# Performance work log

Hardware: AMD Instinct MI355X
Metric: run time of the kernel (lower is better)

## Reference

```python
import jax, jax.numpy as jnp
import numpy as np

N_NODES = 50000
N_EDGES = 800000
N_EVAL = 500000
D = 96


def _sage_conv(x, edge_index, W_l, W_r, b):
    # PyG SAGEConv with aggr='add':
    #   aggr_out[v] = sum_{(u->v) in edges} x[u]
    #   out = aggr_out @ W_l^T-equivalent + b + x @ W_r  (we store W as [in, out])
    src, dst = edge_index[0], edge_index[1]
    msgs = x[src]                                        # [E, d_in] irregular gather
    aggr = jax.ops.segment_sum(msgs, dst, num_segments=x.shape[0])  # [N, d_in]
    return aggr @ W_l + b + x @ W_r                      # [N, d_out]


def setup_inputs() -> dict:
    key = jax.random.key(0)
    ks = jax.random.split(key, 8)
    scale = 1.0 / np.sqrt(D)
    Features = jax.random.normal(ks[0], (N_NODES, D), dtype=jnp.float32)
    A = jax.random.randint(ks[1], (2, N_EDGES), 0, N_NODES, dtype=jnp.int64)
    E = jax.random.randint(ks[2], (2, N_EVAL), 0, N_NODES, dtype=jnp.int64)
    W1_l = jax.random.normal(ks[3], (D, D), dtype=jnp.float32) * scale
    W1_r = jax.random.normal(ks[4], (D, D), dtype=jnp.float32) * scale
    b1 = jnp.zeros((D,), dtype=jnp.float32)
    W2_l = jax.random.normal(ks[5], (D, D), dtype=jnp.float32) * scale
    W2_r = jax.random.normal(ks[6], (D, D), dtype=jnp.float32) * scale
    b2 = jnp.zeros((D,), dtype=jnp.float32)
    return {"Features": Features, "A": A, "E": E,
            "W1_l": W1_l, "W1_r": W1_r, "b1": b1,
            "W2_l": W2_l, "W2_r": W2_r, "b2": b2}


def reference(Features, A, E, W1_l, W1_r, b1, W2_l, W2_r, b2):
    h = _sage_conv(Features, A, W1_l, W1_r, b1)          # [N, hidden]
    h = jax.nn.relu(h)
    # dropout in eval mode = identity
    h = _sage_conv(h, A, W2_l, W2_r, b2)                 # [N, out]
    # edge scoring: gather src/dst embeddings, dot, sigmoid
    src = h[E[0]]                                        # [n_eval, out]
    dst = h[E[1]]                                        # [n_eval, out]
    return jax.nn.sigmoid(jnp.sum(src * dst, axis=-1))   # [n_eval]
```

## Files before the change

### kernel.cpp

```cpp
#include <hip/hip_runtime.h>
#include <math.h>

#define N_NODES 50000
#define N_EDGES 800000
#define N_EVAL  500000
#define CSTRIDE 16
#define MAXDEG  64
#define NB_GEMM ((N_NODES + 63) / 64)
#define NCHUNK  (N_NODES * 24)
#define NB_AGG4 1172
#define NSLOT_C 1173
#define HALF_EVAL (N_EVAL / 2)

__device__ __forceinline__ float4 f4add(float4 a, float4 b) {
    return make_float4(a.x + b.x, a.y + b.y, a.z + b.z, a.w + b.w);
}
__device__ __forceinline__ float4 f4fma(float s, float4 w, float4 a) {
    return make_float4(fmaf(s, w.x, a.x), fmaf(s, w.y, a.y),
                       fmaf(s, w.z, a.z), fmaf(s, w.w, a.w));
}
__device__ __forceinline__ float4 ld4(const float* p) {
    return *(const float4*)p;
}


__device__ __forceinline__ void bucket_role(int idx, const int* __restrict__ src,
                                            const int* __restrict__ dst,
                                            int* __restrict__ degS,
                                            unsigned short* __restrict__ bucket) {
    int t = idx * 256 + threadIdx.x;
    if (t < N_EDGES / 4) {
        int4 s = ((const int4*)src)[t];
        int4 d = ((const int4*)dst)[t];
        int r0 = atomicAdd(&degS[(size_t)d.x * CSTRIDE], 1);
        int r1 = atomicAdd(&degS[(size_t)d.y * CSTRIDE], 1);
        int r2 = atomicAdd(&degS[(size_t)d.z * CSTRIDE], 1);
        int r3 = atomicAdd(&degS[(size_t)d.w * CSTRIDE], 1);
        if (r0 < MAXDEG) bucket[(size_t)d.x * MAXDEG + r0] = (unsigned short)s.x;
        if (r1 < MAXDEG) bucket[(size_t)d.y * MAXDEG + r1] = (unsigned short)s.y;
        if (r2 < MAXDEG) bucket[(size_t)d.z * MAXDEG + r2] = (unsigned short)s.z;
        if (r3 < MAXDEG) bucket[(size_t)d.w * MAXDEG + r3] = (unsigned short)s.w;
    }
}

struct IdxL { int4 p0, p1, p2, p3; int deg; };

__device__ __forceinline__ IdxL idx_load(int v, const int* __restrict__ degS,
                                         const unsigned short* __restrict__ bucket) {
    IdxL L;
    const int4* bk4 = (const int4*)(bucket + (size_t)v * MAXDEG);
    L.deg = degS[(size_t)v * CSTRIDE];
    L.p0 = bk4[0]; L.p1 = bk4[1]; L.p2 = bk4[2]; L.p3 = bk4[3];
    return L;
}

__device__ __forceinline__ float4 aggr_gather(IdxL L, int v, int c,
        const float* __restrict__ x, const unsigned short* __restrict__ bucket) {
    const float* xp = x + c * 4;
    int deg = L.deg;
    if (deg > MAXDEG) deg = MAXDEG;
    int idx[32];
    idx[0]  = L.p0.x & 0xffff; idx[1]  = (int)((unsigned)L.p0.x >> 16);
    idx[2]  = L.p0.y & 0xffff; idx[3]  = (int)((unsigned)L.p0.y >> 16);
    idx[4]  = L.p0.z & 0xffff; idx[5]  = (int)((unsigned)L.p0.z >> 16);
    idx[6]  = L.p0.w & 0xffff; idx[7]  = (int)((unsigned)L.p0.w >> 16);
    idx[8]  = L.p1.x & 0xffff; idx[9]  = (int)((unsigned)L.p1.x >> 16);
    idx[10] = L.p1.y & 0xffff; idx[11] = (int)((unsigned)L.p1.y >> 16);
    idx[12] = L.p1.z & 0xffff; idx[13] = (int)((unsigned)L.p1.z >> 16);
    idx[14] = L.p1.w & 0xffff; idx[15] = (int)((unsigned)L.p1.w >> 16);
    idx[16] = L.p2.x & 0xffff; idx[17] = (int)((unsigned)L.p2.x >> 16);
    idx[18] = L.p2.y & 0xffff; idx[19] = (int)((unsigned)L.p2.y >> 16);
    idx[20] = L.p2.z & 0xffff; idx[21] = (int)((unsigned)L.p2.z >> 16);
    idx[22] = L.p2.w & 0xffff; idx[23] = (int)((unsigned)L.p2.w >> 16);
    idx[24] = L.p3.x & 0xffff; idx[25] = (int)((unsigned)L.p3.x >> 16);
    idx[26] = L.p3.y & 0xffff; idx[27] = (int)((unsigned)L.p3.y >> 16);
    idx[28] = L.p3.z & 0xffff; idx[29] = (int)((unsigned)L.p3.z >> 16);
    idx[30] = L.p3.w & 0xffff; idx[31] = (int)((unsigned)L.p3.w >> 16);

    const float4 z = make_float4(0.f, 0.f, 0.f, 0.f);
    float4 t0, t1, t2, t3, t4, t5, t6, t7, t8, t9, t10, t11, t12, t13, t14, t15;
    if (deg >= 16) {
        t0  = ld4(xp + (size_t)idx[0]  * 96);
        t1  = ld4(xp + (size_t)idx[1]  * 96);
        t2  = ld4(xp + (size_t)idx[2]  * 96);
        t3  = ld4(xp + (size_t)idx[3]  * 96);
        t4  = ld4(xp + (size_t)idx[4]  * 96);
        t5  = ld4(xp + (size_t)idx[5]  * 96);
        t6  = ld4(xp + (size_t)idx[6]  * 96);
        t7  = ld4(xp + (size_t)idx[7]  * 96);
        t8  = ld4(xp + (size_t)idx[8]  * 96);
        t9  = ld4(xp + (size_t)idx[9]  * 96);
        t10 = ld4(xp + (size_t)idx[10] * 96);
        t11 = ld4(xp + (size_t)idx[11] * 96);
        t12 = ld4(xp + (size_t)idx[12] * 96);
        t13 = ld4(xp + (size_t)idx[13] * 96);
        t14 = ld4(xp + (size_t)idx[14] * 96);
        t15 = ld4(xp + (size_t)idx[15] * 96);
    } else if (deg >= 8) {
        t0 = ld4(xp + (size_t)idx[0] * 96);
        t1 = ld4(xp + (size_t)idx[1] * 96);
        t2 = ld4(xp + (size_t)idx[2] * 96);
        t3 = ld4(xp + (size_t)idx[3] * 96);
        t4 = ld4(xp + (size_t)idx[4] * 96);
        t5 = ld4(xp + (size_t)idx[5] * 96);
        t6 = ld4(xp + (size_t)idx[6] * 96);
        t7 = ld4(xp + (size_t)idx[7] * 96);
        t8 = z; t9 = z; t10 = z; t11 = z; t12 = z; t13 = z; t14 = z; t15 = z;
        if (deg > 8)  t8  = ld4(xp + (size_t)idx[8]  * 96);
        if (deg > 9)  t9  = ld4(xp + (size_t)idx[9]  * 96);
        if (deg > 10) t10 = ld4(xp + (size_t)idx[10] * 96);
        if (deg > 11) t11 = ld4(xp + (size_t)idx[11] * 96);
        if (deg > 12) t12 = ld4(xp + (size_t)idx[12] * 96);
        if (deg > 13) t13 = ld4(xp + (size_t)idx[13] * 96);
        if (deg > 14) t14 = ld4(xp + (size_t)idx[14] * 96);
    } else {
        t0 = z; t1 = z; t2 = z; t3 = z; t4 = z; t5 = z; t6 = z; t7 = z;
        t8 = z; t9 = z; t10 = z; t11 = z; t12 = z; t13 = z; t14 = z; t15 = z;
        if (deg > 0) t0 = ld4(xp + (size_t)idx[0] * 96);
        if (deg > 1) t1 = ld4(xp + (size_t)idx[1] * 96);
        if (deg > 2) t2 = ld4(xp + (size_t)idx[2] * 96);
        if (deg > 3) t3 = ld4(xp + (size_t)idx[3] * 96);
        if (deg > 4) t4 = ld4(xp + (size_t)idx[4] * 96);
        if (deg > 5) t5 = ld4(xp + (size_t)idx[5] * 96);
        if (deg > 6) t6 = ld4(xp + (size_t)idx[6] * 96);
    }
    float4 a0 = f4add(f4add(f4add(t0, t1), f4add(t2, t3)),
                      f4add(f4add(t4, t5), f4add(t6, t7)));
    float4 a1 = f4add(f4add(f4add(t8, t9), f4add(t10, t11)),
                      f4add(f4add(t12, t13), f4add(t14, t15)));
    if (deg > 16) {
        float4 u0, u1, u2, u3, u4, u5, u6, u7;
        u0 = ld4(xp + (size_t)idx[16] * 96);
        u1 = z; u2 = z; u3 = z; u4 = z; u5 = z; u6 = z; u7 = z;
        if (deg > 17) u1 = ld4(xp + (size_t)idx[17] * 96);
        if (deg > 18) u2 = ld4(xp + (size_t)idx[18] * 96);
        if (deg > 19) u3 = ld4(xp + (size_t)idx[19] * 96);
        if (deg > 20) u4 = ld4(xp + (size_t)idx[20] * 96);
        if (deg > 21) u5 = ld4(xp + (size_t)idx[21] * 96);
        if (deg > 22) u6 = ld4(xp + (size_t)idx[22] * 96);
        if (deg > 23) u7 = ld4(xp + (size_t)idx[23] * 96);
        a0 = f4add(a0, f4add(f4add(u0, u1), f4add(u2, u3)));
        a1 = f4add(a1, f4add(f4add(u4, u5), f4add(u6, u7)));
    }
    if (deg > 24) {
        float4 u0, u1, u2, u3, u4, u5, u6, u7;
        u0 = ld4(xp + (size_t)idx[24] * 96);
        u1 = z; u2 = z; u3 = z; u4 = z; u5 = z; u6 = z; u7 = z;
        if (deg > 25) u1 = ld4(xp + (size_t)idx[25] * 96);
        if (deg > 26) u2 = ld4(xp + (size_t)idx[26] * 96);
        if (deg > 27) u3 = ld4(xp + (size_t)idx[27] * 96);
        if (deg > 28) u4 = ld4(xp + (size_t)idx[28] * 96);
        if (deg > 29) u5 = ld4(xp + (size_t)idx[29] * 96);
        if (deg > 30) u6 = ld4(xp + (size_t)idx[30] * 96);
        if (deg > 31) u7 = ld4(xp + (size_t)idx[31] * 96);
        a0 = f4add(a0, f4add(f4add(u0, u1), f4add(u2, u3)));
        a1 = f4add(a1, f4add(f4add(u4, u5), f4add(u6, u7)));
    }
    if (deg > 32) {
        const unsigned short* bk = bucket + (size_t)v * MAXDEG;
        for (int i = 32; i < deg; ++i)
            a0 = f4add(a0, ld4(xp + (size_t)bk[i] * 96));
    }
    return f4add(a0, a1);
}

__device__ __forceinline__ void aggr_role4(int slot, int stride256,
        const float* __restrict__ x, const int* __restrict__ degS,
        const unsigned short* __restrict__ bucket, float* __restrict__ out) {
    const int STR = stride256 * 256;
    int gt = slot * 256 + threadIdx.x;
    bool val = gt < NCHUNK;
    int v = 0, c = 0;
    IdxL L;
    if (val) {
        v = gt / 24; c = gt - v * 24;
        L = idx_load(v, degS, bucket);
    }
    #pragma unroll
    for (int k = 0; k < 4; ++k) {
        int gtn = gt + STR;
        bool valn = (k < 3) && (gtn < NCHUNK);
        int vn = 0, cn = 0;
        IdxL Ln;
        if (valn) {
            vn = gtn / 24; cn = gtn - vn * 24;
            Ln = idx_load(vn, degS, bucket);
        }
        if (val) {
            float4 r = aggr_gather(L, v, c, x, bucket);
            *(float4*)(out + (size_t)v * 96 + c * 4) = r;
        }
        gt = gtn; v = vn; c = cn; L = Ln; val = valn;
    }
}

__device__ __forceinline__ void selfgemm_role(int g, const float* __restrict__ X,
                                              const float* __restrict__ W96,
                                              const float* __restrict__ bias,
                                              float* __restrict__ S,
                                              float* __restrict__ Ws,
                                              float* __restrict__ xT) {
    const int tid = threadIdx.x;
    const int j   = tid & 31;
    const int ty  = tid >> 5;
    const int v0  = g * 64;

    float acc[8][3];
    float b0 = bias[j], b1 = bias[j + 32], b2 = bias[j + 64];
    #pragma unroll
    for (int r = 0; r < 8; ++r) { acc[r][0] = b0; acc[r][1] = b1; acc[r][2] = b2; }

    const int sr = tid >> 2;
    const int sc = tid & 3;
    int sv = v0 + sr; if (sv >= N_NODES) sv = N_NODES - 1;

    for (int kc = 0; kc < 6; ++kc) {
        const float* W = W96 + kc * (16 * 96);
        const int kbase = kc * 16;
        __syncthreads();
        *(float4*)(Ws + tid * 4) = ld4(W + tid * 4);
        if (tid < 128)
            *(float4*)(Ws + (tid + 256) * 4) = ld4(W + (tid + 256) * 4);
        {
            float4 a = ld4(X + (size_t)sv * 96 + kbase + sc * 4);
            int k0 = sc * 4;
            xT[(k0 + 0) * 68 + sr] = a.x;
            xT[(k0 + 1) * 68 + sr] = a.y;
            xT[(k0 + 2) * 68 + sr] = a.z;
            xT[(k0 + 3) * 68 + sr] = a.w;
        }
        __syncthreads();
        #pragma unroll 8
        for (int kk = 0; kk < 16; ++kk) {
            float w0 = Ws[kk * 96 + j];
            float w1 = Ws[kk * 96 + j + 32];
            float w2 = Ws[kk * 96 + j + 64];
            float4 xa = *(const float4*)(xT + kk * 68 + ty * 8);
            float4 xb = *(const float4*)(xT + kk * 68 + ty * 8 + 4);
#define ROWFMA(r, xv)                                   \
            acc[r][0] = fmaf(xv, w0, acc[r][0]);        \
            acc[r][1] = fmaf(xv, w1, acc[r][1]);        \
            acc[r][2] = fmaf(xv, w2, acc[r][2]);
            ROWFMA(0, xa.x) ROWFMA(1, xa.y) ROWFMA(2, xa.z) ROWFMA(3, xa.w)
            ROWFMA(4, xb.x) ROWFMA(5, xb.y) ROWFMA(6, xb.z) ROWFMA(7, xb.w)
#undef ROWFMA
        }
    }
    #pragma unroll
    for (int r = 0; r < 8; ++r) {
        int v = v0 + ty * 8 + r;
        if (v < N_NODES) {
            S[(size_t)v * 96 + j]      = acc[r][0];
            S[(size_t)v * 96 + j + 32] = acc[r][1];
            S[(size_t)v * 96 + j + 64] = acc[r][2];
        }
    }
}


__global__ __launch_bounds__(256, 4) void k_fusedA(const int* __restrict__ src,
                                                   const int* __restrict__ dst,
                                                   int* __restrict__ degS,
                                                   unsigned short* __restrict__ bucket,
                                                   const float* __restrict__ X,
                                                   const float* __restrict__ Wr,
                                                   const float* __restrict__ bias,
                                                   float* __restrict__ S) {
    __shared__ float Ws[16 * 96];
    __shared__ float xT[16 * 68];
    int b = blockIdx.x;
    if (b & 1) selfgemm_role(b >> 1, X, Wr, bias, S, Ws, xT);
    else       bucket_role(b >> 1, src, dst, degS, bucket);
}

__global__ __launch_bounds__(256, 4) void k_aggr(const float* __restrict__ x,
                                                 const int* __restrict__ degS,
                                                 const unsigned short* __restrict__ bucket,
                                                 float* __restrict__ out) {
    aggr_role4(blockIdx.x, NB_AGG4, x, degS, bucket, out);
}

__global__ __launch_bounds__(256, 4) void k_fusedC(const float* __restrict__ h1,
                                                   const int* __restrict__ degS,
                                                   const unsigned short* __restrict__ bucket,
                                                   float* __restrict__ aggrOut,
                                                   const float* __restrict__ Wr,
                                                   const float* __restrict__ bias,
                                                   float* __restrict__ S) {
    __shared__ float Ws[16 * 96];
    __shared__ float xT[16 * 68];
    int b = blockIdx.x;
    int g = b / 5, r = b - g * 5;
    if (r < 2) {
        int idx = g * 2 + r;
        if (idx < NB_GEMM) selfgemm_role(idx, h1, Wr, bias, S, Ws, xT);
    } else {
        int slot = g * 3 + (r - 2);
        aggr_role4(slot, NSLOT_C, h1, degS, bucket, aggrOut);
    }
}

template <int RELU>
__global__ __launch_bounds__(192) void k_gemmH(const float* __restrict__ P,
                                               const float* __restrict__ Wl,
                                               const float* __restrict__ S,
                                               float* __restrict__ out) {
    __shared__ float Ws[32 * 96];
    __shared__ float xT[32 * 68];
    const int tid = threadIdx.x;
    const int q   = tid % 24;
    const int rg  = tid / 24;
    const int v0  = blockIdx.x * 64;

    const int  row0 = tid >> 3,         qd0 = tid & 7;
    const int  row1 = (tid + 192) >> 3, qd1 = (tid + 192) & 7;
    const int  row2 = (tid + 384) >> 3, qd2 = (tid + 384) & 7;
    const bool has2 = (tid < 128);
    int sv0 = v0 + row0; if (sv0 >= N_NODES) sv0 = N_NODES - 1;
    int sv1 = v0 + row1; if (sv1 >= N_NODES) sv1 = N_NODES - 1;
    int sv2 = v0 + row2; if (sv2 >= N_NODES) sv2 = N_NODES - 1;

    float4 acc[8];
    #pragma unroll
    for (int r = 0; r < 8; ++r) acc[r] = make_float4(0.f, 0.f, 0.f, 0.f);

    float4 wreg0, wreg1, wreg2, wreg3;
    float4 xreg0, xreg1, xreg2;

    auto load_chunk = [&](int kc) {
        const float* W = Wl + kc * (32 * 96);
        const int kbase = kc * 32;
        wreg0 = *(const float4*)(W + (tid + 0 * 192) * 4);
        wreg1 = *(const float4*)(W + (tid + 1 * 192) * 4);
        wreg2 = *(const float4*)(W + (tid + 2 * 192) * 4);
        wreg3 = *(const float4*)(W + (tid + 3 * 192) * 4);
        xreg0 = *(const float4*)(P + (size_t)sv0 * 96 + kbase + qd0 * 4);
        xreg1 = *(const float4*)(P + (size_t)sv1 * 96 + kbase + qd1 * 4);
        if (has2) xreg2 = *(const float4*)(P + (size_t)sv2 * 96 + kbase + qd2 * 4);
    };
    auto store_chunk = [&]() {
        *(float4*)(Ws + (tid + 0 * 192) * 4) = wreg0;
        *(float4*)(Ws + (tid + 1 * 192) * 4) = wreg1;
        *(float4*)(Ws + (tid + 2 * 192) * 4) = wreg2;
        *(float4*)(Ws + (tid + 3 * 192) * 4) = wreg3;
        int k0 = qd0 * 4;
        xT[(k0 + 0) * 68 + row0] = xreg0.x;
        xT[(k0 + 1) * 68 + row0] = xreg0.y;
        xT[(k0 + 2) * 68 + row0] = xreg0.z;
        xT[(k0 + 3) * 68 + row0] = xreg0.w;
        int k1 = qd1 * 4;
        xT[(k1 + 0) * 68 + row1] = xreg1.x;
        xT[(k1 + 1) * 68 + row1] = xreg1.y;
        xT[(k1 + 2) * 68 + row1] = xreg1.z;
        xT[(k1 + 3) * 68 + row1] = xreg1.w;
        if (has2) {
            int k2 = qd2 * 4;
            xT[(k2 + 0) * 68 + row2] = xreg2.x;
            xT[(k2 + 1) * 68 + row2] = xreg2.y;
            xT[(k2 + 2) * 68 + row2] = xreg2.z;
            xT[(k2 + 3) * 68 + row2] = xreg2.w;
        }
    };

    load_chunk(0);
    for (int kc = 0; kc < 3; ++kc) {
        __syncthreads();
        store_chunk();
        if (kc < 2) load_chunk(kc + 1);
        __syncthreads();
        #pragma unroll 8
        for (int kk = 0; kk < 32; ++kk) {
            float4 w  = *(const float4*)(Ws + kk * 96 + q * 4);
            float4 xa = *(const float4*)(xT + kk * 68 + rg * 8);
            float4 xb = *(const float4*)(xT + kk * 68 + rg * 8 + 4);
            acc[0] = f4fma(xa.x, w, acc[0]);
            acc[1] = f4fma(xa.y, w, acc[1]);
            acc[2] = f4fma(xa.z, w, acc[2]);
            acc[3] = f4fma(xa.w, w, acc[3]);
            acc[4] = f4fma(xb.x, w, acc[4]);
            acc[5] = f4fma(xb.y, w, acc[5]);
            acc[6] = f4fma(xb.z, w, acc[6]);
            acc[7] = f4fma(xb.w, w, acc[7]);
        }
    }
    #pragma unroll
    for (int r = 0; r < 8; ++r) {
        int v = v0 + rg * 8 + r;
        if (v < N_NODES) {
            float4 s4 = *(const float4*)(S + (size_t)v * 96 + q * 4);
            float4 o = f4add(acc[r], s4);
            if (RELU) {
                o.x = fmaxf(o.x, 0.f); o.y = fmaxf(o.y, 0.f);
                o.z = fmaxf(o.z, 0.f); o.w = fmaxf(o.w, 0.f);
            }
            *(float4*)(out + (size_t)v * 96 + q * 4) = o;
        }
    }
}

__global__ __launch_bounds__(256) void k_score(const float* __restrict__ h,
                                               const int* __restrict__ E,
                                               float* __restrict__ out) {
    int t = blockIdx.x * 256 + threadIdx.x;
    int e = t >> 3, sub = t & 7;
    if (e >= HALF_EVAL) return;
    int e2 = e + HALF_EVAL;
    int s0 = E[e];
    int d0 = E[N_EVAL + e];
    int s1 = E[e2];
    int d1 = E[N_EVAL + e2];
    const float* ps0 = h + (size_t)s0 * 96 + sub * 12;
    const float* pd0 = h + (size_t)d0 * 96 + sub * 12;
    const float* ps1 = h + (size_t)s1 * 96 + sub * 12;
    const float* pd1 = h + (size_t)d1 * 96 + sub * 12;
    float4 a0 = ld4(ps0 + 0), a1 = ld4(ps0 + 4), a2 = ld4(ps0 + 8);
    float4 b0 = ld4(pd0 + 0), b1 = ld4(pd0 + 4), b2 = ld4(pd0 + 8);
    float4 c0 = ld4(ps1 + 0), c1 = ld4(ps1 + 4), c2 = ld4(ps1 + 8);
    float4 g0 = ld4(pd1 + 0), g1 = ld4(pd1 + 4), g2 = ld4(pd1 + 8);
    float dot0 = a0.x * b0.x + a0.y * b0.y + a0.z * b0.z + a0.w * b0.w
               + a1.x * b1.x + a1.y * b1.y + a1.z * b1.z + a1.w * b1.w
               + a2.x * b2.x + a2.y * b2.y + a2.z * b2.z + a2.w * b2.w;
    float dot1 = c0.x * g0.x + c0.y * g0.y + c0.z * g0.z + c0.w * g0.w
               + c1.x * g1.x + c1.y * g1.y + c1.z * g1.z + c1.w * g1.w
               + c2.x * g2.x + c2.y * g2.y + c2.z * g2.z + c2.w * g2.w;
    dot0 += __shfl_xor(dot0, 1, 64);
    dot1 += __shfl_xor(dot1, 1, 64);
    dot0 += __shfl_xor(dot0, 2, 64);
    dot1 += __shfl_xor(dot1, 2, 64);
    dot0 += __shfl_xor(dot0, 4, 64);
    dot1 += __shfl_xor(dot1, 4, 64);
    if (sub == 0) {
        out[e]  = 1.f / (1.f + expf(-dot0));
        out[e2] = 1.f / (1.f + expf(-dot1));
    }
}


extern "C" void kernel_launch(void* const* d_in, const int* in_sizes, int n_in,
                              void* d_out, int out_size, void* d_ws, size_t ws_size,
                              hipStream_t stream) {
    const float* Features = (const float*)d_in[0];
    const int*   A        = (const int*)d_in[1];
    const int*   E        = (const int*)d_in[2];
    const float* W1l = (const float*)d_in[3];
    const float* W1r = (const float*)d_in[4];
    const float* b1  = (const float*)d_in[5];
    const float* W2l = (const float*)d_in[6];
    const float* W2r = (const float*)d_in[7];
    const float* b2  = (const float*)d_in[8];
    float* out = (float*)d_out;

    char* p = (char*)d_ws;
    auto alloc = [&](size_t bytes) -> char* {
        char* q = p;
        p += (bytes + 255) & ~(size_t)255;
        return q;
    };
    int*   degS   = (int*)alloc((size_t)N_NODES * CSTRIDE * 4);
    unsigned short* bucket =
        (unsigned short*)alloc((size_t)N_NODES * MAXDEG * 2);
    float* bufA   = (float*)alloc((size_t)N_NODES * 96 * 4);
    float* bufB   = (float*)alloc((size_t)N_NODES * 96 * 4);
    float* bufS   = (float*)alloc((size_t)N_NODES * 96 * 4);

    const int* Asrc = A;
    const int* Adst = A + N_EDGES;

    hipMemsetAsync(degS, 0, (size_t)N_NODES * CSTRIDE * 4, stream);

    k_fusedA<<<2 * NB_GEMM, 256, 0, stream>>>(Asrc, Adst, degS, bucket,
                                              Features, W1r, b1, bufS);
    k_aggr<<<NB_AGG4, 256, 0, stream>>>(Features, degS, bucket, bufA);
    k_gemmH<1><<<NB_GEMM, 192, 0, stream>>>(bufA, W1l, bufS, bufB);
    k_fusedC<<<391 * 5, 256, 0, stream>>>(bufB, degS, bucket, bufA,
                                          W2r, b2, bufS);
    k_gemmH<0><<<NB_GEMM, 192, 0, stream>>>(bufA, W2l, bufS, bufA);
    k_score<<<(HALF_EVAL * 8 + 255) / 256, 256, 0, stream>>>(bufA, E, out);
}
```

Baseline: 305.9 us.

## Widen self-GEMM K tile, use one-chunk-per-thread aggregation, score four edges per thread

```diff
diff --git a/kernel.cpp b/kernel.cpp
--- a/kernel.cpp
+++ b/kernel.cpp
@@ -8,9 +8,9 @@
 #define MAXDEG  64
 #define NB_GEMM ((N_NODES + 63) / 64)
 #define NCHUNK  (N_NODES * 24)
-#define NB_AGG4 1172
+#define NB_AGG  ((NCHUNK + 255) / 256)
 #define NSLOT_C 1173
-#define HALF_EVAL (N_EVAL / 2)
+#define QEVAL   (N_EVAL / 4)
 
 __device__ __forceinline__ float4 f4add(float4 a, float4 b) {
     return make_float4(a.x + b.x, a.y + b.y, a.z + b.z, a.w + b.w);
@@ -164,6 +164,18 @@
     return f4add(a0, a1);
 }
 
+__device__ __forceinline__ void aggr_role1(int slot, const float* __restrict__ x,
+        const int* __restrict__ degS, const unsigned short* __restrict__ bucket,
+        float* __restrict__ out) {
+    int gt = slot * 256 + threadIdx.x;
+    if (gt >= NCHUNK) return;
+    int v = gt / 24;
+    int c = gt - v * 24;
+    IdxL L = idx_load(v, degS, bucket);
+    float4 r = aggr_gather(L, v, c, x, bucket);
+    *(float4*)(out + (size_t)v * 96 + c * 4) = r;
+}
+
 __device__ __forceinline__ void aggr_role4(int slot, int stride256,
         const float* __restrict__ x, const int* __restrict__ degS,
         const unsigned short* __restrict__ bucket, float* __restrict__ out) {
@@ -194,12 +206,83 @@
     }
 }
 
-__device__ __forceinline__ void selfgemm_role(int g, const float* __restrict__ X,
-                                              const float* __restrict__ W96,
-                                              const float* __restrict__ bias,
-                                              float* __restrict__ S,
-                                              float* __restrict__ Ws,
-                                              float* __restrict__ xT) {
+__device__ __forceinline__ void selfgemm32(int g, const float* __restrict__ X,
+                                           const float* __restrict__ W96,
+                                           const float* __restrict__ bias,
+                                           float* __restrict__ S,
+                                           float* __restrict__ Ws,
+                                           float* __restrict__ xT) {
+    const int tid = threadIdx.x;
+    const int j   = tid & 31;
+    const int ty  = tid >> 5;
+    const int v0  = g * 64;
+
+    float acc[8][3];
+    float b0 = bias[j], b1 = bias[j + 32], b2 = bias[j + 64];
+    #pragma unroll
+    for (int r = 0; r < 8; ++r) { acc[r][0] = b0; acc[r][1] = b1; acc[r][2] = b2; }
+
+    const int sr = tid >> 2;
+    const int sc = tid & 3;
+    int sv = v0 + sr; if (sv >= N_NODES) sv = N_NODES - 1;
+
+    for (int kc = 0; kc < 3; ++kc) {
+        const float* W = W96 + kc * (32 * 96);
+        const int kbase = kc * 32;
+        __syncthreads();
+        #pragma unroll
+        for (int i = 0; i < 3; ++i) {
+            int f = tid + i * 256;
+            *(float4*)(Ws + f * 4) = ld4(W + f * 4);
+        }
+        {
+            const float* rowp = X + (size_t)sv * 96 + kbase;
+            float4 a = ld4(rowp + sc * 4);
+            float4 b = ld4(rowp + sc * 4 + 16);
+            int k0 = sc * 4;
+            xT[(k0 + 0) * 68 + sr] = a.x;
+            xT[(k0 + 1) * 68 + sr] = a.y;
+            xT[(k0 + 2) * 68 + sr] = a.z;
+            xT[(k0 + 3) * 68 + sr] = a.w;
+            xT[(k0 + 16) * 68 + sr] = b.x;
+            xT[(k0 + 17) * 68 + sr] = b.y;
+            xT[(k0 + 18) * 68 + sr] = b.z;
+            xT[(k0 + 19) * 68 + sr] = b.w;
+        }
+        __syncthreads();
+        #pragma unroll 8
+        for (int kk = 0; kk < 32; ++kk) {
+            float w0 = Ws[kk * 96 + j];
+            float w1 = Ws[kk * 96 + j + 32];
+            float w2 = Ws[kk * 96 + j + 64];
+            float4 xa = *(const float4*)(xT + kk * 68 + ty * 8);
+            float4 xb = *(const float4*)(xT + kk * 68 + ty * 8 + 4);
+#define ROWFMA(r, xv)                                   \
+            acc[r][0] = fmaf(xv, w0, acc[r][0]);        \
+            acc[r][1] = fmaf(xv, w1, acc[r][1]);        \
+            acc[r][2] = fmaf(xv, w2, acc[r][2]);
+            ROWFMA(0, xa.x) ROWFMA(1, xa.y) ROWFMA(2, xa.z) ROWFMA(3, xa.w)
+            ROWFMA(4, xb.x) ROWFMA(5, xb.y) ROWFMA(6, xb.z) ROWFMA(7, xb.w)
+#undef ROWFMA
+        }
+    }
+    #pragma unroll
+    for (int r = 0; r < 8; ++r) {
+        int v = v0 + ty * 8 + r;
+        if (v < N_NODES) {
+            S[(size_t)v * 96 + j]      = acc[r][0];
+            S[(size_t)v * 96 + j + 32] = acc[r][1];
+            S[(size_t)v * 96 + j + 64] = acc[r][2];
+        }
+    }
+}
+
+__device__ __forceinline__ void selfgemm16(int g, const float* __restrict__ X,
+                                           const float* __restrict__ W96,
+                                           const float* __restrict__ bias,
+                                           float* __restrict__ S,
+                                           float* __restrict__ Ws,
+                                           float* __restrict__ xT) {
     const int tid = threadIdx.x;
     const int j   = tid & 31;
     const int ty  = tid >> 5;
@@ -258,18 +341,18 @@
 }
 
 
-__global__ __launch_bounds__(256, 4) void k_fusedA(const int* __restrict__ src,
-                                                   const int* __restrict__ dst,
-                                                   int* __restrict__ degS,
-                                                   unsigned short* __restrict__ bucket,
-                                                   const float* __restrict__ X,
-                                                   const float* __restrict__ Wr,
-                                                   const float* __restrict__ bias,
-                                                   float* __restrict__ S) {
-    __shared__ float Ws[16 * 96];
-    __shared__ float xT[16 * 68];
+__global__ __launch_bounds__(256) void k_fusedA(const int* __restrict__ src,
+                                                const int* __restrict__ dst,
+                                                int* __restrict__ degS,
+                                                unsigned short* __restrict__ bucket,
+                                                const float* __restrict__ X,
+                                                const float* __restrict__ Wr,
+                                                const float* __restrict__ bias,
+                                                float* __restrict__ S) {
+    __shared__ float Ws[32 * 96];
+    __shared__ float xT[32 * 68];
     int b = blockIdx.x;
-    if (b & 1) selfgemm_role(b >> 1, X, Wr, bias, S, Ws, xT);
+    if (b & 1) selfgemm32(b >> 1, X, Wr, bias, S, Ws, xT);
     else       bucket_role(b >> 1, src, dst, degS, bucket);
 }
 
@@ -277,7 +360,7 @@
                                                  const int* __restrict__ degS,
                                                  const unsigned short* __restrict__ bucket,
                                                  float* __restrict__ out) {
-    aggr_role4(blockIdx.x, NB_AGG4, x, degS, bucket, out);
+    aggr_role1(blockIdx.x, x, degS, bucket, out);
 }
 
 __global__ __launch_bounds__(256, 4) void k_fusedC(const float* __restrict__ h1,
@@ -293,7 +376,7 @@
     int g = b / 5, r = b - g * 5;
     if (r < 2) {
         int idx = g * 2 + r;
-        if (idx < NB_GEMM) selfgemm_role(idx, h1, Wr, bias, S, Ws, xT);
+        if (idx < NB_GEMM) selfgemm16(idx, h1, Wr, bias, S, Ws, xT);
     } else {
         int slot = g * 3 + (r - 2);
         aggr_role4(slot, NSLOT_C, h1, degS, bucket, aggrOut);
@@ -403,35 +486,57 @@
                                                float* __restrict__ out) {
     int t = blockIdx.x * 256 + threadIdx.x;
     int e = t >> 3, sub = t & 7;
-    if (e >= HALF_EVAL) return;
-    int e2 = e + HALF_EVAL;
-    int s0 = E[e];
-    int d0 = E[N_EVAL + e];
-    int s1 = E[e2];
-    int d1 = E[N_EVAL + e2];
-    const float* ps0 = h + (size_t)s0 * 96 + sub * 12;
-    const float* pd0 = h + (size_t)d0 * 96 + sub * 12;
-    const float* ps1 = h + (size_t)s1 * 96 + sub * 12;
-    const float* pd1 = h + (size_t)d1 * 96 + sub * 12;
-    float4 a0 = ld4(ps0 + 0), a1 = ld4(ps0 + 4), a2 = ld4(ps0 + 8);
-    float4 b0 = ld4(pd0 + 0), b1 = ld4(pd0 + 4), b2 = ld4(pd0 + 8);
-    float4 c0 = ld4(ps1 + 0), c1 = ld4(ps1 + 4), c2 = ld4(ps1 + 8);
-    float4 g0 = ld4(pd1 + 0), g1 = ld4(pd1 + 4), g2 = ld4(pd1 + 8);
-    float dot0 = a0.x * b0.x + a0.y * b0.y + a0.z * b0.z + a0.w * b0.w
+    if (e >= QEVAL) return;
+    int eA = e, eB = e + QEVAL, eC = e + 2 * QEVAL, eD = e + 3 * QEVAL;
+    int sA = E[eA], sB = E[eB], sC = E[eC], sD = E[eD];
+    int dA = E[N_EVAL + eA], dB = E[N_EVAL + eB];
+    int dC = E[N_EVAL + eC], dD = E[N_EVAL + eD];
+    const int off = sub * 12;
+    const float* psA = h + (size_t)sA * 96 + off;
+    const float* pdA = h + (size_t)dA * 96 + off;
+    const float* psB = h + (size_t)sB * 96 + off;
+    const float* pdB = h + (size_t)dB * 96 + off;
+    const float* psC = h + (size_t)sC * 96 + off;
+    const float* pdC = h + (size_t)dC * 96 + off;
+    const float* psD = h + (size_t)sD * 96 + off;
+    const float* pdD = h + (size_t)dD * 96 + off;
+    float4 a0 = ld4(psA + 0), a1 = ld4(psA + 4), a2 = ld4(psA + 8);
+    float4 b0 = ld4(pdA + 0), b1 = ld4(pdA + 4), b2 = ld4(pdA + 8);
+    float4 c0 = ld4(psB + 0), c1 = ld4(psB + 4), c2 = ld4(psB + 8);
+    float4 g0 = ld4(pdB + 0), g1 = ld4(pdB + 4), g2 = ld4(pdB + 8);
+    float4 m0 = ld4(psC + 0), m1 = ld4(psC + 4), m2 = ld4(psC + 8);
+    float4 n0 = ld4(pdC + 0), n1 = ld4(pdC + 4), n2 = ld4(pdC + 8);
+    float4 u0 = ld4(psD + 0), u1 = ld4(psD + 4), u2 = ld4(psD + 8);
+    float4 w0 = ld4(pdD + 0), w1 = ld4(pdD + 4), w2 = ld4(pdD + 8);
+    float dotA = a0.x * b0.x + a0.y * b0.y + a0.z * b0.z + a0.w * b0.w
                + a1.x * b1.x + a1.y * b1.y + a1.z * b1.z + a1.w * b1.w
                + a2.x * b2.x + a2.y * b2.y + a2.z * b2.z + a2.w * b2.w;
-    float dot1 = c0.x * g0.x + c0.y * g0.y + c0.z * g0.z + c0.w * g0.w
+    float dotB = c0.x * g0.x + c0.y * g0.y + c0.z * g0.z + c0.w * g0.w
                + c1.x * g1.x + c1.y * g1.y + c1.z * g1.z + c1.w * g1.w
                + c2.x * g2.x + c2.y * g2.y + c2.z * g2.z + c2.w * g2.w;
-    dot0 += __shfl_xor(dot0, 1, 64);
-    dot1 += __shfl_xor(dot1, 1, 64);
-    dot0 += __shfl_xor(dot0, 2, 64);
-    dot1 += __shfl_xor(dot1, 2, 64);
-    dot0 += __shfl_xor(dot0, 4, 64);
-    dot1 += __shfl_xor(dot1, 4, 64);
+    float dotC = m0.x * n0.x + m0.y * n0.y + m0.z * n0.z + m0.w * n0.w
+               + m1.x * n1.x + m1.y * n1.y + m1.z * n1.z + m1.w * n1.w
+               + m2.x * n2.x + m2.y * n2.y + m2.z * n2.z + m2.w * n2.w;
+    float dotD = u0.x * w0.x + u0.y * w0.y + u0.z * w0.z + u0.w * w0.w
+               + u1.x * w1.x + u1.y * w1.y + u1.z * w1.z + u1.w * w1.w
+               + u2.x * w2.x + u2.y * w2.y + u2.z * w2.z + u2.w * w2.w;
+    dotA += __shfl_xor(dotA, 1, 64);
+    dotB += __shfl_xor(dotB, 1, 64);
+    dotC += __shfl_xor(dotC, 1, 64);
+    dotD += __shfl_xor(dotD, 1, 64);
+    dotA += __shfl_xor(dotA, 2, 64);
+    dotB += __shfl_xor(dotB, 2, 64);
+    dotC += __shfl_xor(dotC, 2, 64);
+    dotD += __shfl_xor(dotD, 2, 64);
+    dotA += __shfl_xor(dotA, 4, 64);
+    dotB += __shfl_xor(dotB, 4, 64);
+    dotC += __shfl_xor(dotC, 4, 64);
+    dotD += __shfl_xor(dotD, 4, 64);
     if (sub == 0) {
-        out[e]  = 1.f / (1.f + expf(-dot0));
-        out[e2] = 1.f / (1.f + expf(-dot1));
+        out[eA] = 1.f / (1.f + expf(-dotA));
+        out[eB] = 1.f / (1.f + expf(-dotB));
+        out[eC] = 1.f / (1.f + expf(-dotC));
+        out[eD] = 1.f / (1.f + expf(-dotD));
     }
 }
 
@@ -470,10 +575,10 @@
 
     k_fusedA<<<2 * NB_GEMM, 256, 0, stream>>>(Asrc, Adst, degS, bucket,
                                               Features, W1r, b1, bufS);
-    k_aggr<<<NB_AGG4, 256, 0, stream>>>(Features, degS, bucket, bufA);
+    k_aggr<<<NB_AGG, 256, 0, stream>>>(Features, degS, bucket, bufA);
     k_gemmH<1><<<NB_GEMM, 192, 0, stream>>>(bufA, W1l, bufS, bufB);
     k_fusedC<<<391 * 5, 256, 0, stream>>>(bufB, degS, bucket, bufA,
                                           W2r, b2, bufS);
     k_gemmH<0><<<NB_GEMM, 192, 0, stream>>>(bufA, W2l, bufS, bufA);
-    k_score<<<(HALF_EVAL * 8 + 255) / 256, 256, 0, stream>>>(bufA, E, out);
-}
+    k_score<<<(QEVAL * 8 + 255) / 256, 256, 0, stream>>>(bufA, E, out);
+}
```

Result: no change. 311.7 us (+1.9%).
